# Optimization experiments

Measured on AMD Instinct MI355X. Metric: run time of the kernel, lower is better.

## Reference

```python
import jax, jax.numpy as jnp
import numpy as np

N_HEADS = 32
N_KV_HEADS = 8
HEAD_DIM = 128
DIM = N_HEADS * HEAD_DIM          # 4096
KV_DIM = N_KV_HEADS * HEAD_DIM    # 1024
N_REP = N_HEADS // N_KV_HEADS     # 4
MAX_SEQ = 4096
T = 1
POS = MAX_SEQ - T                 # decode last position


def _rope_tables(max_seq, head_dim, theta=10000.0):
    inv = 1.0 / (theta ** (np.arange(0, head_dim, 2, dtype=np.float32) / head_dim))
    ang = np.arange(max_seq, dtype=np.float32)[:, None] * inv[None, :]  # [S, D/2]
    return jnp.asarray(np.cos(ang)), jnp.asarray(np.sin(ang))


def setup_inputs() -> dict:
    key = jax.random.key(0)
    ks = jax.random.split(key, 8)
    w = 0.02
    cos, sin = _rope_tables(MAX_SEQ, HEAD_DIM)
    return {
        "x": jax.random.normal(ks[0], (1, T, DIM), dtype=jnp.float32),
        "freqs_cos": cos,
        "freqs_sin": sin,
        "k_buf": jax.random.normal(ks[1], (1, N_KV_HEADS, MAX_SEQ, HEAD_DIM), dtype=jnp.float32),
        "v_buf": jax.random.normal(ks[2], (1, N_KV_HEADS, MAX_SEQ, HEAD_DIM), dtype=jnp.float32),
        "wq": jax.random.normal(ks[3], (DIM, DIM), dtype=jnp.float32) * w,
        "wk": jax.random.normal(ks[4], (KV_DIM, DIM), dtype=jnp.float32) * w,
        "wv": jax.random.normal(ks[5], (KV_DIM, DIM), dtype=jnp.float32) * w,
        "wo": jax.random.normal(ks[6], (DIM, DIM), dtype=jnp.float32) * w,
        "pos": POS,
    }


def _apply_rotary(x, cos, sin):
    # x: [B, H, T, D]; cos/sin: [T, D/2]; interleaved-pair complex rotation
    xr = x.reshape(*x.shape[:-1], HEAD_DIM // 2, 2)
    x0, x1 = xr[..., 0], xr[..., 1]
    c = cos[None, None, :, :]
    s = sin[None, None, :, :]
    o0 = x0 * c - x1 * s
    o1 = x0 * s + x1 * c
    return jnp.stack([o0, o1], axis=-1).reshape(x.shape)


def reference(x, freqs_cos, freqs_sin, k_buf, v_buf, wq, wk, wv, wo, pos):
    B, Tq, _ = x.shape
    q = (x @ wq.T).reshape(B, Tq, N_HEADS, HEAD_DIM).transpose(0, 2, 1, 3)
    k = (x @ wk.T).reshape(B, Tq, N_KV_HEADS, HEAD_DIM).transpose(0, 2, 1, 3)
    v = (x @ wv.T).reshape(B, Tq, N_KV_HEADS, HEAD_DIM).transpose(0, 2, 1, 3)

    cos = freqs_cos[pos:pos + Tq]
    sin = freqs_sin[pos:pos + Tq]
    q = _apply_rotary(q, cos, sin)
    k = _apply_rotary(k, cos, sin)

    # static KV-cache write (pos is a Python int -> static slice)
    k_buf = jax.lax.dynamic_update_slice(k_buf, k, (0, 0, pos, 0))
    v_buf = jax.lax.dynamic_update_slice(v_buf, v, (0, 0, pos, 0))
    k_all = k_buf[:, :, :pos + Tq]   # [B, n_kv, S, D]
    v_all = v_buf[:, :, :pos + Tq]

    # GQA: repeat_interleave kv heads to n_heads
    k_all = jnp.repeat(k_all, N_REP, axis=1)
    v_all = jnp.repeat(v_all, N_REP, axis=1)

    scale = 1.0 / np.sqrt(HEAD_DIM).astype(np.float32)
    scores = jnp.einsum('bhtd,bhsd->bhts', q, k_all) * scale
    attn = jax.nn.softmax(scores, axis=-1)          # decode path: no mask, not causal
    out = jnp.einsum('bhts,bhsd->bhtd', attn, v_all)
    out = out.transpose(0, 2, 1, 3).reshape(B, Tq, DIM)
    return out @ wo.T
```

## Files before the change

kernel.cpp:

```cpp
#include <hip/hip_runtime.h>
#include <math.h>

#define NHEADS 32
#define NKV 8
#define HD 128
#define DIM 4096
#define KV_DIM 1024
#define SEQ 4096
#define POS 4095
#define NCHUNK 64
#define CHUNK 64
#define PPOS 16

#define WS_QROT   0
#define WS_KNEW   4096
#define WS_VNEW   5120
#define WS_L      6144
#define WS_ACC    8192
#define WS_AOUT   270336

__device__ __forceinline__ float dot4(float4 a, float4 b) {
    return a.x * b.x + a.y * b.y + a.z * b.z + a.w * b.w;
}

template <int CTRL>
__device__ __forceinline__ float dppadd(float x) {
    return x + __int_as_float(__builtin_amdgcn_update_dpp(
        0, __float_as_int(x), CTRL, 0xF, 0xF, true));
}

__global__ __launch_bounds__(256) void qkv_kernel(
    const float* __restrict__ x,
    const float* __restrict__ wq, const float* __restrict__ wk,
    const float* __restrict__ wv,
    const float* __restrict__ fc, const float* __restrict__ fs,
    float* __restrict__ ws)
{
    __shared__ float xs[DIM];
    {
        const float4* x4 = (const float4*)x;
        float4* xs4 = (float4*)xs;
        #pragma unroll
        for (int u = 0; u < 4; ++u)
            xs4[u * 256 + threadIdx.x] = x4[u * 256 + threadIdx.x];
    }
    __syncthreads();

    const int wave = threadIdx.x >> 6;
    const int lane = threadIdx.x & 63;
    const int row0 = (blockIdx.x * 4 + wave) * 2;

    const float4* xs4 = (const float4*)xs;
    float res[2];
    #pragma unroll
    for (int r = 0; r < 2; ++r) {
        const int row = row0 + r;
        const float* wrow;
        if (row < DIM)               wrow = wq + (size_t)row * DIM;
        else if (row < DIM + KV_DIM) wrow = wk + (size_t)(row - DIM) * DIM;
        else                         wrow = wv + (size_t)(row - DIM - KV_DIM) * DIM;
        const float4* w4 = (const float4*)wrow;

        float4 wb[16];
        #pragma unroll
        for (int u = 0; u < 16; ++u) wb[u] = w4[u * 64 + lane];

        float acc = 0.f;
        #pragma unroll
        for (int u = 0; u < 16; ++u) acc += dot4(wb[u], xs4[u * 64 + lane]);

        #pragma unroll
        for (int off = 32; off; off >>= 1) acc += __shfl_xor(acc, off);
        res[r] = acc;
    }

    if (lane == 0) {
        if (row0 < DIM + KV_DIM) {
            const int p = (row0 & (HD - 1)) >> 1;
            const float c = fc[POS * (HD / 2) + p];
            const float s = fs[POS * (HD / 2) + p];
            ws[row0]     = res[0] * c - res[1] * s;
            ws[row0 + 1] = res[0] * s + res[1] * c;
        } else {
            ws[row0]     = res[0];
            ws[row0 + 1] = res[1];
        }
    }
}

__global__ __launch_bounds__(256) void attn_partial(
    const float* __restrict__ kbuf, const float* __restrict__ vbuf,
    float* __restrict__ ws)
{
    const float* qrot = ws + WS_QROT;
    const float* knew = ws + WS_KNEW;
    const float* vnew = ws + WS_VNEW;
    float* l_arr   = ws + WS_L;
    float* acc_arr = ws + WS_ACC;

    const int g     = blockIdx.y;
    const int chunk = blockIdx.x;
    const int wave  = threadIdx.x >> 6;
    const int lane  = threadIdx.x & 63;
    const int qg    = lane >> 4;
    const int ql    = lane & 15;
    const int s0    = chunk * CHUNK + wave * PPOS;

    float4 q0[4], q1[4];
    #pragma unroll
    for (int h = 0; h < 4; ++h) {
        const float4* qb = (const float4*)(qrot + (size_t)(4 * g + h) * HD);
        q0[h] = qb[ql];
        q1[h] = qb[ql + 16];
    }

    const float scale = 0.08838834764831845f;
    float lsum[4] = {0.f, 0.f, 0.f, 0.f};
    float4 acc0[4] = {}, acc1[4] = {};

    float4 kb0[2], kb1[2], vb0[2], vb1[2];
    {
        const int s = s0 + qg;
        const float* kr = (s == POS) ? (knew + g * HD) : (kbuf + ((size_t)g * SEQ + s) * HD);
        const float* vr = (s == POS) ? (vnew + g * HD) : (vbuf + ((size_t)g * SEQ + s) * HD);
        kb0[0] = ((const float4*)kr)[ql]; kb1[0] = ((const float4*)kr)[ql + 16];
        vb0[0] = ((const float4*)vr)[ql]; vb1[0] = ((const float4*)vr)[ql + 16];
    }

    #pragma unroll
    for (int it = 0; it < PPOS / 4; ++it) {
        if (it + 1 < PPOS / 4) {
            const int s = s0 + (it + 1) * 4 + qg;
            const float* kr = (s == POS) ? (knew + g * HD) : (kbuf + ((size_t)g * SEQ + s) * HD);
            const float* vr = (s == POS) ? (vnew + g * HD) : (vbuf + ((size_t)g * SEQ + s) * HD);
            const int nb = (it + 1) & 1;
            kb0[nb] = ((const float4*)kr)[ql]; kb1[nb] = ((const float4*)kr)[ql + 16];
            vb0[nb] = ((const float4*)vr)[ql]; vb1[nb] = ((const float4*)vr)[ql + 16];
        }
        const int b = it & 1;

        float d[4];
        #pragma unroll
        for (int h = 0; h < 4; ++h)
            d[h] = dot4(kb0[b], q0[h]) + dot4(kb1[b], q1[h]);

        #pragma unroll
        for (int h = 0; h < 4; ++h) {
            d[h] = dppadd<0xB1>(d[h]);
            d[h] = dppadd<0x4E>(d[h]);
            d[h] = dppadd<0x124>(d[h]);
            d[h] = dppadd<0x128>(d[h]);
        }

        #pragma unroll
        for (int h = 0; h < 4; ++h) {
            const float p = __expf(d[h] * scale - 8.0f);
            lsum[h] += p;
            acc0[h].x += p * vb0[b].x;
            acc0[h].y += p * vb0[b].y;
            acc0[h].z += p * vb0[b].z;
            acc0[h].w += p * vb0[b].w;
            acc1[h].x += p * vb1[b].x;
            acc1[h].y += p * vb1[b].y;
            acc1[h].z += p * vb1[b].z;
            acc1[h].w += p * vb1[b].w;
        }
    }

    #pragma unroll
    for (int h = 0; h < 4; ++h) {
        lsum[h] += __shfl_xor(lsum[h], 16);
        lsum[h] += __shfl_xor(lsum[h], 32);
        acc0[h].x += __shfl_xor(acc0[h].x, 16); acc0[h].x += __shfl_xor(acc0[h].x, 32);
        acc0[h].y += __shfl_xor(acc0[h].y, 16); acc0[h].y += __shfl_xor(acc0[h].y, 32);
        acc0[h].z += __shfl_xor(acc0[h].z, 16); acc0[h].z += __shfl_xor(acc0[h].z, 32);
        acc0[h].w += __shfl_xor(acc0[h].w, 16); acc0[h].w += __shfl_xor(acc0[h].w, 32);
        acc1[h].x += __shfl_xor(acc1[h].x, 16); acc1[h].x += __shfl_xor(acc1[h].x, 32);
        acc1[h].y += __shfl_xor(acc1[h].y, 16); acc1[h].y += __shfl_xor(acc1[h].y, 32);
        acc1[h].z += __shfl_xor(acc1[h].z, 16); acc1[h].z += __shfl_xor(acc1[h].z, 32);
        acc1[h].w += __shfl_xor(acc1[h].w, 16); acc1[h].w += __shfl_xor(acc1[h].w, 32);
    }

    __shared__ float sacc[4][4][HD];
    __shared__ float sl[4][4];
    if (qg == 0) {
        #pragma unroll
        for (int h = 0; h < 4; ++h) {
            ((float4*)sacc[wave][h])[ql]      = acc0[h];
            ((float4*)sacc[wave][h])[ql + 16] = acc1[h];
        }
    }
    if (lane == 0) {
        #pragma unroll
        for (int h = 0; h < 4; ++h) sl[wave][h] = lsum[h];
    }
    __syncthreads();

    for (int idx = threadIdx.x; idx < 4 * HD; idx += 256) {
        const int h = idx >> 7, j = idx & (HD - 1);
        const float s = sacc[0][h][j] + sacc[1][h][j] + sacc[2][h][j] + sacc[3][h][j];
        acc_arr[((size_t)(4 * g + h) * NCHUNK + chunk) * HD + j] = s;
    }
    if (threadIdx.x < 4) {
        const int h = threadIdx.x;
        l_arr[(4 * g + h) * NCHUNK + chunk] = sl[0][h] + sl[1][h] + sl[2][h] + sl[3][h];
    }
}

__global__ __launch_bounds__(256) void attn_combine(float* __restrict__ ws)
{
    const float* l_arr   = ws + WS_L;
    const float* acc_arr = ws + WS_ACC;
    float* aout = ws + WS_AOUT;

    const int h = blockIdx.x;
    const int t = threadIdx.x;
    const int j = t & (HD - 1);
    const int half = t >> 7;

    __shared__ float part[256];
    __shared__ float sInvL;

    float sum = 0.f;
    const int c0 = half * (NCHUNK / 2);
    #pragma unroll 8
    for (int c = 0; c < NCHUNK / 2; ++c)
        sum += acc_arr[((size_t)h * NCHUNK + c0 + c) * HD + j];
    part[t] = sum;
    __syncthreads();

    if (t < 64) {
        float lv = l_arr[h * NCHUNK + t];
        #pragma unroll
        for (int off = 32; off; off >>= 1) lv += __shfl_xor(lv, off);
        if (t == 0) sInvL = 1.f / lv;
    }
    __syncthreads();

    if (t < HD) aout[h * HD + t] = (part[t] + part[t + 128]) * sInvL;
}

__global__ __launch_bounds__(256) void out_kernel(
    const float* __restrict__ wo, const float* __restrict__ ws,
    float* __restrict__ out)
{
    __shared__ float as[DIM];
    {
        const float4* a4 = (const float4*)(ws + WS_AOUT);
        float4* as4 = (float4*)as;
        #pragma unroll
        for (int u = 0; u < 4; ++u)
            as4[u * 256 + threadIdx.x] = a4[u * 256 + threadIdx.x];
    }
    __syncthreads();

    const int wave = threadIdx.x >> 6;
    const int lane = threadIdx.x & 63;
    const int row  = blockIdx.x * 4 + wave;

    const float4* w4  = (const float4*)(wo + (size_t)row * DIM);
    const float4* as4 = (const float4*)as;

    float4 wb[16];
    #pragma unroll
    for (int u = 0; u < 16; ++u) wb[u] = w4[u * 64 + lane];

    float acc = 0.f;
    #pragma unroll
    for (int u = 0; u < 16; ++u) acc += dot4(wb[u], as4[u * 64 + lane]);

    #pragma unroll
    for (int off = 32; off; off >>= 1) acc += __shfl_xor(acc, off);
    if (lane == 0) out[row] = acc;
}

extern "C" void kernel_launch(void* const* d_in, const int* in_sizes, int n_in,
                              void* d_out, int out_size, void* d_ws, size_t ws_size,
                              hipStream_t stream)
{
    const float* x    = (const float*)d_in[0];
    const float* fc   = (const float*)d_in[1];
    const float* fs   = (const float*)d_in[2];
    const float* kbuf = (const float*)d_in[3];
    const float* vbuf = (const float*)d_in[4];
    const float* wq   = (const float*)d_in[5];
    const float* wk   = (const float*)d_in[6];
    const float* wv   = (const float*)d_in[7];
    const float* wo   = (const float*)d_in[8];

    float* ws  = (float*)d_ws;
    float* out = (float*)d_out;

    qkv_kernel<<<(DIM + 2 * KV_DIM) / 8, 256, 0, stream>>>(x, wq, wk, wv, fc, fs, ws);
    attn_partial<<<dim3(NCHUNK, NKV), 256, 0, stream>>>(kbuf, vbuf, ws);
    attn_combine<<<NHEADS, 256, 0, stream>>>(ws);
    out_kernel<<<DIM / 4, 256, 0, stream>>>(wo, ws, out);
}
```

Measured before the change: 42.63 us.

## Replace split-KV combine kernel with atomic accumulation and fold normalization into output projection

Attention partial blocks now atomically add their per-chunk accumulators and softmax denominators into small global buffers instead of writing per-chunk partials. The separate combine kernel is removed, and the 1/l normalization is applied when out_kernel loads the attention output into shared memory. Buffers are zeroed at the start of the QKV kernel. This removes a launch and a large partial-buffer round trip, at the cost of atomic contention and nondeterministic float summation order.

```diff
diff --git a/kernel.cpp b/kernel.cpp
--- a/kernel.cpp
+++ b/kernel.cpp
@@ -15,9 +15,8 @@
 #define WS_QROT   0
 #define WS_KNEW   4096
 #define WS_VNEW   5120
-#define WS_L      6144
-#define WS_ACC    8192
-#define WS_AOUT   270336
+#define WS_ACCS   6144
+#define WS_LSUM   10240
 
 __device__ __forceinline__ float dot4(float4 a, float4 b) {
     return a.x * b.x + a.y * b.y + a.z * b.z + a.w * b.w;
@@ -36,6 +35,11 @@
     const float* __restrict__ fc, const float* __restrict__ fs,
     float* __restrict__ ws)
 {
+    if (blockIdx.x < 16) {
+        ws[WS_ACCS + blockIdx.x * 256 + threadIdx.x] = 0.f;
+        if (blockIdx.x == 0 && threadIdx.x < NHEADS) ws[WS_LSUM + threadIdx.x] = 0.f;
+    }
+
     __shared__ float xs[DIM];
     {
         const float4* x4 = (const float4*)x;
@@ -95,8 +99,8 @@
     const float* qrot = ws + WS_QROT;
     const float* knew = ws + WS_KNEW;
     const float* vnew = ws + WS_VNEW;
-    float* l_arr   = ws + WS_L;
-    float* acc_arr = ws + WS_ACC;
+    float* accs = ws + WS_ACCS;
+    float* lsg  = ws + WS_LSUM;
 
     const int g     = blockIdx.y;
     const int chunk = blockIdx.x;
@@ -198,46 +202,13 @@
 
     for (int idx = threadIdx.x; idx < 4 * HD; idx += 256) {
         const int h = idx >> 7, j = idx & (HD - 1);
-        const float s = sacc[0][h][j] + sacc[1][h][j] + sacc[2][h][j] + sacc[3][h][j];
-        acc_arr[((size_t)(4 * g + h) * NCHUNK + chunk) * HD + j] = s;
+        const float sv = sacc[0][h][j] + sacc[1][h][j] + sacc[2][h][j] + sacc[3][h][j];
+        atomicAdd(&accs[(4 * g + h) * HD + j], sv);
     }
     if (threadIdx.x < 4) {
         const int h = threadIdx.x;
-        l_arr[(4 * g + h) * NCHUNK + chunk] = sl[0][h] + sl[1][h] + sl[2][h] + sl[3][h];
-    }
-}
-
-__global__ __launch_bounds__(256) void attn_combine(float* __restrict__ ws)
-{
-    const float* l_arr   = ws + WS_L;
-    const float* acc_arr = ws + WS_ACC;
-    float* aout = ws + WS_AOUT;
-
-    const int h = blockIdx.x;
-    const int t = threadIdx.x;
-    const int j = t & (HD - 1);
-    const int half = t >> 7;
-
-    __shared__ float part[256];
-    __shared__ float sInvL;
-
-    float sum = 0.f;
-    const int c0 = half * (NCHUNK / 2);
-    #pragma unroll 8
-    for (int c = 0; c < NCHUNK / 2; ++c)
-        sum += acc_arr[((size_t)h * NCHUNK + c0 + c) * HD + j];
-    part[t] = sum;
-    __syncthreads();
-
-    if (t < 64) {
-        float lv = l_arr[h * NCHUNK + t];
-        #pragma unroll
-        for (int off = 32; off; off >>= 1) lv += __shfl_xor(lv, off);
-        if (t == 0) sInvL = 1.f / lv;
-    }
-    __syncthreads();
-
-    if (t < HD) aout[h * HD + t] = (part[t] + part[t + 128]) * sInvL;
+        atomicAdd(&lsg[4 * g + h], sl[0][h] + sl[1][h] + sl[2][h] + sl[3][h]);
+    }
 }
 
 __global__ __launch_bounds__(256) void out_kernel(
@@ -245,12 +216,23 @@
     float* __restrict__ out)
 {
     __shared__ float as[DIM];
+    __shared__ float sinv[NHEADS];
+
+    if (threadIdx.x < NHEADS)
+        sinv[threadIdx.x] = 1.f / ws[WS_LSUM + threadIdx.x];
+    __syncthreads();
+
     {
-        const float4* a4 = (const float4*)(ws + WS_AOUT);
+        const float4* a4 = (const float4*)(ws + WS_ACCS);
         float4* as4 = (float4*)as;
         #pragma unroll
-        for (int u = 0; u < 4; ++u)
-            as4[u * 256 + threadIdx.x] = a4[u * 256 + threadIdx.x];
+        for (int u = 0; u < 4; ++u) {
+            const int j4 = u * 256 + threadIdx.x;
+            float4 v = a4[j4];
+            const float iv = sinv[j4 >> 5];
+            v.x *= iv; v.y *= iv; v.z *= iv; v.w *= iv;
+            as4[j4] = v;
+        }
     }
     __syncthreads();
 
@@ -293,6 +275,5 @@
 
     qkv_kernel<<<(DIM + 2 * KV_DIM) / 8, 256, 0, stream>>>(x, wq, wk, wv, fc, fs, ws);
     attn_partial<<<dim3(NCHUNK, NKV), 256, 0, stream>>>(kbuf, vbuf, ws);
-    attn_combine<<<NHEADS, 256, 0, stream>>>(ws);
     out_kernel<<<DIM / 4, 256, 0, stream>>>(wo, ws, out);
 }
```

New measurement: 42.72 us, median of 3. No clear change (+0.2%).
